# Performance work log

Measured on AMD Instinct MI355X. Metric: run time of the kernel, lower is better.

The kernel has to match this reference:

```python
import jax, jax.numpy as jnp
import numpy as np

N_NODES = 40000


def gcn_conv(x, edge_index, W, b, num_nodes):
    """PyG GCNConv: add self-loops, sym-normalize, x @ W.T then scatter-add, + bias."""
    src = edge_index[0]
    dst = edge_index[1]
    loop = jnp.arange(num_nodes, dtype=src.dtype)
    src = jnp.concatenate([src, loop])
    dst = jnp.concatenate([dst, loop])
    # linear transform first (PyG applies lin before propagate)
    h = x @ W.T  # [N, out]
    # symmetric normalization: deg over destination (with self-loops)
    deg = jax.ops.segment_sum(jnp.ones_like(dst, dtype=h.dtype), dst, num_segments=num_nodes)
    dinv = jnp.where(deg > 0, jax.lax.rsqrt(deg), 0.0)
    norm = dinv[src] * dinv[dst]  # [E+N]
    msg = h[src] * norm[:, None]  # gather + scale
    out = jax.ops.segment_sum(msg, dst, num_segments=num_nodes)  # scatter-add
    return out + b


def setup_inputs() -> dict:
    key = jax.random.key(0)
    k1, k2, k3, k4, k5, k6, k7 = jax.random.split(key, 7)
    C, H, F_out = 128, 128, 1
    E = 640000
    x = jax.random.normal(k1, (N_NODES, C), dtype=jnp.float32)
    edge_index = jax.random.randint(k2, (2, E), 0, N_NODES, dtype=jnp.int64)
    # Glorot-ish init for conv weights (PyG lin.weight shape [out, in]), zero bias
    W1 = jax.random.normal(k3, (H, C), dtype=jnp.float32) / np.sqrt(C)
    b1 = jnp.zeros((H,), dtype=jnp.float32)
    W2 = jax.random.normal(k4, (F_out, H), dtype=jnp.float32) / np.sqrt(H)
    b2 = jnp.zeros((F_out,), dtype=jnp.float32)
    return {"x": x, "edge_index": edge_index, "W1": W1, "b1": b1, "W2": W2, "b2": b2}


def reference(x, edge_index, W1, b1, W2, b2):
    h = gcn_conv(x, edge_index, W1, b1, N_NODES)
    h = jax.nn.relu(h)
    out = gcn_conv(h, edge_index, W2, b2, N_NODES)
    return jax.nn.sigmoid(out)
```

## Files before the change

### kernel.cpp

```cpp
#include <hip/hip_runtime.h>
#include <math.h>
#include <stdint.h>

#define FDIM 128
#define CAP  48
#define H8SCALE 8.0f

typedef __bf16 bf16x8 __attribute__((ext_vector_type(8)));
typedef float  f32x4  __attribute__((ext_vector_type(4)));
typedef float  f32x2  __attribute__((ext_vector_type(2)));

__device__ __forceinline__ ushort f2bf(float f) {
    uint32_t u = __float_as_uint(f);
    uint32_t r = (u >> 16) & 1;
    return (ushort)((u + 0x7fffu + r) >> 16);
}
__device__ __forceinline__ bf16x8 pack8(float4 a, float4 b) {
    union { uint32_t q[4]; bf16x8 v; } u;
    u.q[0] = (uint32_t)f2bf(a.x) | ((uint32_t)f2bf(a.y) << 16);
    u.q[1] = (uint32_t)f2bf(a.z) | ((uint32_t)f2bf(a.w) << 16);
    u.q[2] = (uint32_t)f2bf(b.x) | ((uint32_t)f2bf(b.y) << 16);
    u.q[3] = (uint32_t)f2bf(b.z) | ((uint32_t)f2bf(b.w) << 16);
    return u.v;
}


__global__ __launch_bounds__(256) void k_prep(const float* __restrict__ W,
                                              const float* __restrict__ W2,
                                              const float* __restrict__ b1,
                                              ushort* __restrict__ Wb,
                                              float* __restrict__ W2p,
                                              float* __restrict__ b1p,
                                              int4* __restrict__ cnt4, int n4) {
    int t = blockIdx.x * blockDim.x + threadIdx.x;
    if (t < 2048) {
        int lane = t & 63, f = t >> 6;
        int jblk = f >> 2, ks = f & 3;
        int row = jblk * 16 + (lane & 15);
        int col = ks * 32 + (lane >> 4) * 8;
        const float* p = W + (size_t)row * FDIM + col;
        float4 v0 = *(const float4*)p;
        float4 v1 = *(const float4*)(p + 4);
        union { bf16x8 v; uint4 q; } u;
        u.v = pack8(v0, v1);
        *(uint4*)(Wb + (size_t)t * 8) = u.q;
    } else if (t < 2176) {
        int i = t - 2048;
        int q = i >> 2, tt = i & 3;
        int c = 64 * (q >> 4) + 16 * tt + (q & 15);
        W2p[i] = W2[c];
        b1p[i] = b1[c];
    } else {
        int z = t - 2176;
        if (z < n4) cnt4[z] = make_int4(0, 0, 0, 0);
    }
}


__global__ __launch_bounds__(256) void k_scatter_ell(const int* __restrict__ src,
                                                     const int* __restrict__ dst,
                                                     int* __restrict__ cnt,
                                                     ushort* __restrict__ ell, int E) {
    int e = blockIdx.x * blockDim.x + threadIdx.x;
    if (e < E) {
        int d = dst[e];
        int p = atomicAdd(&cnt[d], 1);
        if (p < CAP) ell[(size_t)d * CAP + p] = (ushort)src[e];
    }
}


__global__ __launch_bounds__(256) void k_linear(const float* __restrict__ x,
                                                const ushort* __restrict__ Wb,
                                                const int* __restrict__ cnt,
                                                uint32_t* __restrict__ h8, int n) {
    int tid = threadIdx.x;
    int lane = tid & 63, wid = tid >> 6;
    int mg = wid >> 1, jg2 = wid & 1;
    int node0 = (int)blockIdx.x * 64;
    int m0 = mg * 32;
    int lrow = lane & 15, kg = lane >> 4;

#pragma unroll
    for (int mt = 0; mt < 2; ++mt) {
        int row = node0 + m0 + mt * 16 + lrow;
        bool ok = (row < n);
        float s = ok ? rsqrtf((float)cnt[row] + 1.0f) : 0.f;
        const float* rp = x + (size_t)row * FDIM;
        bf16x8 af[4];
#pragma unroll
        for (int ks = 0; ks < 4; ++ks) {
            float4 v0 = make_float4(0.f, 0.f, 0.f, 0.f), v1 = v0;
            if (ok) {
                const float* p = rp + ks * 32 + kg * 8;
                v0 = *(const float4*)p;
                v1 = *(const float4*)(p + 4);
            }
            v0.x *= s; v0.y *= s; v0.z *= s; v0.w *= s;
            v1.x *= s; v1.y *= s; v1.z *= s; v1.w *= s;
            af[ks] = pack8(v0, v1);
        }
        f32x4 acc[4] = {};
#pragma unroll
        for (int jt = 0; jt < 4; ++jt) {
            int jblk = jg2 * 4 + jt;
#pragma unroll
            for (int ks = 0; ks < 4; ++ks) {
                bf16x8 bfr = *(const bf16x8*)(Wb + ((size_t)(jblk * 4 + ks) * 64 + lane) * 8);
                acc[jt] = __builtin_amdgcn_mfma_f32_16x16x32_bf16(af[ks], bfr, acc[jt], 0, 0, 0);
            }
        }
#pragma unroll
        for (int r = 0; r < 4; ++r) {
            int gi = node0 + m0 + mt * 16 + kg * 4 + r;
            if (gi < n) {
                int u = __builtin_amdgcn_cvt_pk_fp8_f32(acc[0][r] * H8SCALE,
                                                        acc[1][r] * H8SCALE, 0, false);
                u = __builtin_amdgcn_cvt_pk_fp8_f32(acc[2][r] * H8SCALE,
                                                    acc[3][r] * H8SCALE, u, true);
                h8[(size_t)gi * 32 + jg2 * 16 + lrow] = (uint32_t)u;
            }
        }
    }
}


__global__ __launch_bounds__(256) void k_agg1_h2(const uint32_t* __restrict__ h8,
                                                 const ushort* __restrict__ ell,
                                                 const int* __restrict__ cnt,
                                                 const float* __restrict__ b1p,
                                                 const float* __restrict__ W2p,
                                                 float* __restrict__ h2s, int n) {
    int gtid = blockIdx.x * blockDim.x + threadIdx.x;
    int wv = gtid >> 6;
    int lane = threadIdx.x & 63;
    int qw = (lane >> 4);
    int l = lane & 15;
    int d = wv * 4 + qw;
    if (d >= n) return;

    int degt = cnt[d];
    int deg = min(degt, CAP);
    int idx0 = (l < deg) ? (int)ell[(size_t)d * CAP + l] : 0;
    int idx1 = (16 + l < deg) ? (int)ell[(size_t)d * CAP + 16 + l] : 0;
    int idx2 = (32 + l < deg) ? (int)ell[(size_t)d * CAP + 32 + l] : 0;

    float a[8];
    {
        uint2 u = *(const uint2*)(h8 + (size_t)d * 32 + l * 2);
        f32x2 p0 = __builtin_amdgcn_cvt_pk_f32_fp8((int)u.x, false);
        f32x2 q0 = __builtin_amdgcn_cvt_pk_f32_fp8((int)u.x, true);
        f32x2 p1 = __builtin_amdgcn_cvt_pk_f32_fp8((int)u.y, false);
        f32x2 q1 = __builtin_amdgcn_cvt_pk_f32_fp8((int)u.y, true);
        a[0] = p0[0]; a[1] = p0[1]; a[2] = q0[0]; a[3] = q0[1];
        a[4] = p1[0]; a[5] = p1[1]; a[6] = q1[0]; a[7] = q1[1];
    }

    int k = 0;
    for (; k + 3 < deg; k += 4) {
        uint2 v[4];
#pragma unroll
        for (int r = 0; r < 4; ++r) {
            int kk = k + r;
            int base = (kk < 16) ? idx0 : ((kk < 32) ? idx1 : idx2);
            int s = __shfl(base, kk & 15, 16);
            v[r] = *(const uint2*)(h8 + (size_t)s * 32 + l * 2);
        }
#pragma unroll
        for (int r = 0; r < 4; ++r) {
            f32x2 p0 = __builtin_amdgcn_cvt_pk_f32_fp8((int)v[r].x, false);
            f32x2 q0 = __builtin_amdgcn_cvt_pk_f32_fp8((int)v[r].x, true);
            f32x2 p1 = __builtin_amdgcn_cvt_pk_f32_fp8((int)v[r].y, false);
            f32x2 q1 = __builtin_amdgcn_cvt_pk_f32_fp8((int)v[r].y, true);
            a[0] += p0[0]; a[1] += p0[1]; a[2] += q0[0]; a[3] += q0[1];
            a[4] += p1[0]; a[5] += p1[1]; a[6] += q1[0]; a[7] += q1[1];
        }
    }
    for (; k < deg; ++k) {
        int base = (k < 16) ? idx0 : ((k < 32) ? idx1 : idx2);
        int s = __shfl(base, k & 15, 16);
        uint2 u = *(const uint2*)(h8 + (size_t)s * 32 + l * 2);
        f32x2 p0 = __builtin_amdgcn_cvt_pk_f32_fp8((int)u.x, false);
        f32x2 q0 = __builtin_amdgcn_cvt_pk_f32_fp8((int)u.x, true);
        f32x2 p1 = __builtin_amdgcn_cvt_pk_f32_fp8((int)u.y, false);
        f32x2 q1 = __builtin_amdgcn_cvt_pk_f32_fp8((int)u.y, true);
        a[0] += p0[0]; a[1] += p0[1]; a[2] += q0[0]; a[3] += q0[1];
        a[4] += p1[0]; a[5] += p1[1]; a[6] += q1[0]; a[7] += q1[1];
    }

    float dd = rsqrtf((float)degt + 1.0f);
    float sc = dd * (1.0f / H8SCALE);
    float4 bb0 = *(const float4*)(b1p + l * 8);
    float4 bb1 = *(const float4*)(b1p + l * 8 + 4);
    float4 ww0 = *(const float4*)(W2p + l * 8);
    float4 ww1 = *(const float4*)(W2p + l * 8 + 4);
    float s = fmaxf(a[0] * sc + bb0.x, 0.f) * ww0.x + fmaxf(a[1] * sc + bb0.y, 0.f) * ww0.y +
              fmaxf(a[2] * sc + bb0.z, 0.f) * ww0.z + fmaxf(a[3] * sc + bb0.w, 0.f) * ww0.w +
              fmaxf(a[4] * sc + bb1.x, 0.f) * ww1.x + fmaxf(a[5] * sc + bb1.y, 0.f) * ww1.y +
              fmaxf(a[6] * sc + bb1.z, 0.f) * ww1.z + fmaxf(a[7] * sc + bb1.w, 0.f) * ww1.w;
#pragma unroll
    for (int o = 8; o; o >>= 1) s += __shfl_down(s, o, 16);
    if (l == 0) h2s[d] = s * dd;
}


__global__ __launch_bounds__(256) void k_agg2(const float* __restrict__ h2s,
                                              const ushort* __restrict__ ell,
                                              const int* __restrict__ cnt,
                                              const float* __restrict__ b2,
                                              float* __restrict__ out, int n) {
    int gtid = blockIdx.x * blockDim.x + threadIdx.x;
    int i = gtid >> 6;
    int lane = threadIdx.x & 63;
    if (i >= n) return;

    int degt = cnt[i];
    int deg = min(degt, CAP);
    float v = 0.f;
    if (lane < deg) {
        int s = ell[(size_t)i * CAP + lane];
        v = h2s[s];
    }
#pragma unroll
    for (int o = 32; o; o >>= 1) v += __shfl_down(v, o);
    if (lane == 0) {
        float dd = rsqrtf((float)degt + 1.0f);
        float r = (h2s[i] + v) * dd + b2[0];
        out[i] = 1.f / (1.f + expf(-r));
    }
}


extern "C" void kernel_launch(void* const* d_in, const int* in_sizes, int n_in,
                              void* d_out, int out_size, void* d_ws, size_t ws_size,
                              hipStream_t stream) {
    const float* x  = (const float*)d_in[0];
    const int*   ei = (const int*)d_in[1];
    const float* W1 = (const float*)d_in[2];
    const float* b1 = (const float*)d_in[3];
    const float* W2 = (const float*)d_in[4];
    const float* b2 = (const float*)d_in[5];

    int n = out_size;
    int E = in_sizes[1] / 2;
    const int* src = ei;
    const int* dst = ei + E;

    char* w = (char*)d_ws;
    int*      cnt = (int*)w;      w += (size_t)((n + 3) & ~3) * 4;
    ushort*   Wb  = (ushort*)w;   w += (size_t)2048 * 8 * 2;
    float*    W2p = (float*)w;    w += 128 * 4;
    float*    b1p = (float*)w;    w += 128 * 4;
    ushort*   ell = (ushort*)w;   w += (size_t)n * CAP * 2;
    uint32_t* h8  = (uint32_t*)w; w += (size_t)n * 32 * 4;
    float*    h2s = (float*)w;    w += (size_t)n * 4;

    int n4 = ((n + 3) & ~3) / 4;

    k_prep<<<(2176 + n4 + 255) / 256, 256, 0, stream>>>(W1, W2, b1, Wb, W2p, b1p,
                                                        (int4*)cnt, n4);
    k_scatter_ell<<<(E + 255) / 256, 256, 0, stream>>>(src, dst, cnt, ell, E);
    k_linear<<<(n + 63) / 64, 256, 0, stream>>>(x, Wb, cnt, h8, n);
    k_agg1_h2<<<(n * 16 + 255) / 256, 256, 0, stream>>>(h8, ell, cnt, b1p, W2p, h2s, n);
    k_agg2<<<(n * 64 + 255) / 256, 256, 0, stream>>>(h2s, ell, cnt, b2, (float*)d_out, n);
}
```

Before: 76.93 us.

## Remap aggregation kernels to 8 lanes per node with wider loads

The first aggregation kernel now assigns 8 lanes per destination node instead of 16. Each lane loads 16 fp8 features as a uint4, and the lanes read neighbor indices directly from the ELL row instead of broadcasting them through shuffles. The loop is unrolled by 8 to keep more gathers in flight. The second aggregation uses 8 lanes per node, each summing up to 6 neighbors, instead of a full 64-lane wave per node, which cuts idle lanes and the length of the reduction. The trade-off is more registers and redundant index loads within each node's lane group.

After: 74.01 us. 1.04x faster.

```diff
diff --git a/kernel.cpp b/kernel.cpp
--- a/kernel.cpp
+++ b/kernel.cpp
@@ -125,6 +125,17 @@
 }
 
 
+__device__ __forceinline__ void acc16(float* a, uint4 v) {
+#pragma unroll
+    for (int j = 0; j < 4; ++j) {
+        uint32_t w = (&v.x)[j];
+        f32x2 p = __builtin_amdgcn_cvt_pk_f32_fp8((int)w, false);
+        f32x2 q = __builtin_amdgcn_cvt_pk_f32_fp8((int)w, true);
+        a[4 * j + 0] += p[0]; a[4 * j + 1] += p[1];
+        a[4 * j + 2] += q[0]; a[4 * j + 3] += q[1];
+    }
+}
+
 __global__ __launch_bounds__(256) void k_agg1_h2(const uint32_t* __restrict__ h8,
                                                  const ushort* __restrict__ ell,
                                                  const int* __restrict__ cnt,
@@ -134,72 +145,60 @@
     int gtid = blockIdx.x * blockDim.x + threadIdx.x;
     int wv = gtid >> 6;
     int lane = threadIdx.x & 63;
-    int qw = (lane >> 4);
-    int l = lane & 15;
-    int d = wv * 4 + qw;
+    int ew = lane >> 3;
+    int l = lane & 7;
+    int d = wv * 8 + ew;
     if (d >= n) return;
 
     int degt = cnt[d];
     int deg = min(degt, CAP);
-    int idx0 = (l < deg) ? (int)ell[(size_t)d * CAP + l] : 0;
-    int idx1 = (16 + l < deg) ? (int)ell[(size_t)d * CAP + 16 + l] : 0;
-    int idx2 = (32 + l < deg) ? (int)ell[(size_t)d * CAP + 32 + l] : 0;
-
-    float a[8];
-    {
-        uint2 u = *(const uint2*)(h8 + (size_t)d * 32 + l * 2);
-        f32x2 p0 = __builtin_amdgcn_cvt_pk_f32_fp8((int)u.x, false);
-        f32x2 q0 = __builtin_amdgcn_cvt_pk_f32_fp8((int)u.x, true);
-        f32x2 p1 = __builtin_amdgcn_cvt_pk_f32_fp8((int)u.y, false);
-        f32x2 q1 = __builtin_amdgcn_cvt_pk_f32_fp8((int)u.y, true);
-        a[0] = p0[0]; a[1] = p0[1]; a[2] = q0[0]; a[3] = q0[1];
-        a[4] = p1[0]; a[5] = p1[1]; a[6] = q1[0]; a[7] = q1[1];
-    }
+    const ushort* row = ell + (size_t)d * CAP;
+
+    float a[16] = {};
+    acc16(a, *(const uint4*)(h8 + (size_t)d * 32 + l * 4));
 
     int k = 0;
+    for (; k + 7 < deg; k += 8) {
+        int s[8];
+#pragma unroll
+        for (int r = 0; r < 8; ++r) s[r] = (int)row[k + r];
+        uint4 v[8];
+#pragma unroll
+        for (int r = 0; r < 8; ++r)
+            v[r] = *(const uint4*)(h8 + (size_t)s[r] * 32 + l * 4);
+#pragma unroll
+        for (int r = 0; r < 8; ++r) acc16(a, v[r]);
+    }
     for (; k + 3 < deg; k += 4) {
-        uint2 v[4];
-#pragma unroll
-        for (int r = 0; r < 4; ++r) {
-            int kk = k + r;
-            int base = (kk < 16) ? idx0 : ((kk < 32) ? idx1 : idx2);
-            int s = __shfl(base, kk & 15, 16);
-            v[r] = *(const uint2*)(h8 + (size_t)s * 32 + l * 2);
-        }
-#pragma unroll
-        for (int r = 0; r < 4; ++r) {
-            f32x2 p0 = __builtin_amdgcn_cvt_pk_f32_fp8((int)v[r].x, false);
-            f32x2 q0 = __builtin_amdgcn_cvt_pk_f32_fp8((int)v[r].x, true);
-            f32x2 p1 = __builtin_amdgcn_cvt_pk_f32_fp8((int)v[r].y, false);
-            f32x2 q1 = __builtin_amdgcn_cvt_pk_f32_fp8((int)v[r].y, true);
-            a[0] += p0[0]; a[1] += p0[1]; a[2] += q0[0]; a[3] += q0[1];
-            a[4] += p1[0]; a[5] += p1[1]; a[6] += q1[0]; a[7] += q1[1];
-        }
+        int s[4];
+#pragma unroll
+        for (int r = 0; r < 4; ++r) s[r] = (int)row[k + r];
+        uint4 v[4];
+#pragma unroll
+        for (int r = 0; r < 4; ++r)
+            v[r] = *(const uint4*)(h8 + (size_t)s[r] * 32 + l * 4);
+#pragma unroll
+        for (int r = 0; r < 4; ++r) acc16(a, v[r]);
     }
     for (; k < deg; ++k) {
-        int base = (k < 16) ? idx0 : ((k < 32) ? idx1 : idx2);
-        int s = __shfl(base, k & 15, 16);
-        uint2 u = *(const uint2*)(h8 + (size_t)s * 32 + l * 2);
-        f32x2 p0 = __builtin_amdgcn_cvt_pk_f32_fp8((int)u.x, false);
-        f32x2 q0 = __builtin_amdgcn_cvt_pk_f32_fp8((int)u.x, true);
-        f32x2 p1 = __builtin_amdgcn_cvt_pk_f32_fp8((int)u.y, false);
-        f32x2 q1 = __builtin_amdgcn_cvt_pk_f32_fp8((int)u.y, true);
-        a[0] += p0[0]; a[1] += p0[1]; a[2] += q0[0]; a[3] += q0[1];
-        a[4] += p1[0]; a[5] += p1[1]; a[6] += q1[0]; a[7] += q1[1];
+        int s = (int)row[k];
+        acc16(a, *(const uint4*)(h8 + (size_t)s * 32 + l * 4));
     }
 
     float dd = rsqrtf((float)degt + 1.0f);
     float sc = dd * (1.0f / H8SCALE);
-    float4 bb0 = *(const float4*)(b1p + l * 8);
-    float4 bb1 = *(const float4*)(b1p + l * 8 + 4);
-    float4 ww0 = *(const float4*)(W2p + l * 8);
-    float4 ww1 = *(const float4*)(W2p + l * 8 + 4);
-    float s = fmaxf(a[0] * sc + bb0.x, 0.f) * ww0.x + fmaxf(a[1] * sc + bb0.y, 0.f) * ww0.y +
-              fmaxf(a[2] * sc + bb0.z, 0.f) * ww0.z + fmaxf(a[3] * sc + bb0.w, 0.f) * ww0.w +
-              fmaxf(a[4] * sc + bb1.x, 0.f) * ww1.x + fmaxf(a[5] * sc + bb1.y, 0.f) * ww1.y +
-              fmaxf(a[6] * sc + bb1.z, 0.f) * ww1.z + fmaxf(a[7] * sc + bb1.w, 0.f) * ww1.w;
-#pragma unroll
-    for (int o = 8; o; o >>= 1) s += __shfl_down(s, o, 16);
+    float s = 0.f;
+#pragma unroll
+    for (int j = 0; j < 4; ++j) {
+        float4 bb = *(const float4*)(b1p + l * 16 + j * 4);
+        float4 ww = *(const float4*)(W2p + l * 16 + j * 4);
+        s += fmaxf(a[4 * j + 0] * sc + bb.x, 0.f) * ww.x +
+             fmaxf(a[4 * j + 1] * sc + bb.y, 0.f) * ww.y +
+             fmaxf(a[4 * j + 2] * sc + bb.z, 0.f) * ww.z +
+             fmaxf(a[4 * j + 3] * sc + bb.w, 0.f) * ww.w;
+    }
+#pragma unroll
+    for (int o = 4; o; o >>= 1) s += __shfl_down(s, o, 8);
     if (l == 0) h2s[d] = s * dd;
 }
 
@@ -210,20 +209,32 @@
                                               const float* __restrict__ b2,
                                               float* __restrict__ out, int n) {
     int gtid = blockIdx.x * blockDim.x + threadIdx.x;
-    int i = gtid >> 6;
+    int wv = gtid >> 6;
     int lane = threadIdx.x & 63;
+    int ew = lane >> 3;
+    int l = lane & 7;
+    int i = wv * 8 + ew;
     if (i >= n) return;
 
     int degt = cnt[i];
     int deg = min(degt, CAP);
+    const ushort* row = ell + (size_t)i * CAP;
+    int s0 = (l < deg)      ? (int)row[l]      : -1;
+    int s1 = (8 + l < deg)  ? (int)row[8 + l]  : -1;
+    int s2 = (16 + l < deg) ? (int)row[16 + l] : -1;
+    int s3 = (24 + l < deg) ? (int)row[24 + l] : -1;
+    int s4 = (32 + l < deg) ? (int)row[32 + l] : -1;
+    int s5 = (40 + l < deg) ? (int)row[40 + l] : -1;
     float v = 0.f;
-    if (lane < deg) {
-        int s = ell[(size_t)i * CAP + lane];
-        v = h2s[s];
-    }
-#pragma unroll
-    for (int o = 32; o; o >>= 1) v += __shfl_down(v, o);
-    if (lane == 0) {
+    if (s0 >= 0) v += h2s[s0];
+    if (s1 >= 0) v += h2s[s1];
+    if (s2 >= 0) v += h2s[s2];
+    if (s3 >= 0) v += h2s[s3];
+    if (s4 >= 0) v += h2s[s4];
+    if (s5 >= 0) v += h2s[s5];
+#pragma unroll
+    for (int o = 4; o; o >>= 1) v += __shfl_down(v, o, 8);
+    if (l == 0) {
         float dd = rsqrtf((float)degt + 1.0f);
         float r = (h2s[i] + v) * dd + b2[0];
         out[i] = 1.f / (1.f + expf(-r));
@@ -261,6 +272,6 @@
                                                         (int4*)cnt, n4);
     k_scatter_ell<<<(E + 255) / 256, 256, 0, stream>>>(src, dst, cnt, ell, E);
     k_linear<<<(n + 63) / 64, 256, 0, stream>>>(x, Wb, cnt, h8, n);
-    k_agg1_h2<<<(n * 16 + 255) / 256, 256, 0, stream>>>(h8, ell, cnt, b1p, W2p, h2s, n);
-    k_agg2<<<(n * 64 + 255) / 256, 256, 0, stream>>>(h2s, ell, cnt, b2, (float*)d_out, n);
-}
+    k_agg1_h2<<<(n * 8 + 255) / 256, 256, 0, stream>>>(h8, ell, cnt, b1p, W2p, h2s, n);
+    k_agg2<<<(n * 8 + 255) / 256, 256, 0, stream>>>(h2s, ell, cnt, b2, (float*)d_out, n);
+}
```
